# Performance work log

Measured on AMD Instinct MI355X. Metric: run time of the kernel, lower is better.

## Reference

```python
import jax, jax.numpy as jnp
import numpy as np


def _resize_bilinear_ac(img, out_h, out_w):
    """Bilinear resize with align_corners=True. img: [B, C, Hin, Win]."""
    B, C, Hin, Win = img.shape
    ys = jnp.linspace(0.0, Hin - 1.0, out_h)
    xs = jnp.linspace(0.0, Win - 1.0, out_w)
    y0 = jnp.floor(ys).astype(jnp.int32)
    x0 = jnp.floor(xs).astype(jnp.int32)
    y1 = jnp.clip(y0 + 1, 0, Hin - 1)
    x1 = jnp.clip(x0 + 1, 0, Win - 1)
    wy = (ys - y0.astype(ys.dtype))[:, None]   # [out_h, 1]
    wx = (xs - x0.astype(xs.dtype))[None, :]   # [1, out_w]
    g = lambda yi, xi: img[:, :, yi[:, None], xi[None, :]]  # [B,C,out_h,out_w]
    top = (1.0 - wx) * g(y0, x0) + wx * g(y0, x1)
    bot = (1.0 - wx) * g(y1, x0) + wx * g(y1, x1)
    return (1.0 - wy) * top + wy * bot


def setup_inputs() -> dict:
    key = jax.random.key(0)
    k1, k2, k3, k4 = jax.random.split(key, 4)
    B, C, H, W = 4, 2048, 48, 48
    x = jax.random.normal(k1, (B, C, H, W), jnp.float32)
    cam = jax.random.normal(k2, (B, 384, 384), jnp.float32)
    # xavier-uniform 1x1 conv weights: bound = sqrt(6/(fan_in+fan_out))
    bound = float(np.sqrt(6.0 / (C + C)))
    Wq = jax.random.uniform(k3, (C, C), jnp.float32, -bound, bound)
    Wk = jax.random.uniform(k4, (C, C), jnp.float32, -bound, bound)
    bq = jnp.zeros((C,), jnp.float32)
    bk = jnp.zeros((C,), jnp.float32)
    gamma = jnp.ones((1,), jnp.float32)
    return {"x": x, "cam": cam, "Wq": Wq, "bq": bq, "Wk": Wk, "bk": bk, "gamma": gamma}


def reference(x, cam, Wq, bq, Wk, bk, gamma):
    B, C, H, W = x.shape
    N = H * W
    # cam[cam == 255] = 0
    cam = jnp.where(cam == 255.0, 0.0, cam)
    cam_r = _resize_bilinear_ac(cam[:, None, :, :], H, W)      # [B,1,H,W]
    mask = (cam_r > 0).astype(x.dtype).reshape(B, 1, N).transpose(0, 2, 1)  # [B,N,1]
    # 1x1 convs == per-pixel matmul over channels
    q = jnp.einsum('bchw,oc->bohw', x, Wq) + bq[None, :, None, None]
    k = jnp.einsum('bchw,oc->bohw', x, Wk) + bk[None, :, None, None]
    q = q.reshape(B, C, N).transpose(0, 2, 1)   # [B,N,C]
    k = k.reshape(B, C, N)                       # [B,C,N]
    energy = jnp.einsum('bnc,bcm->bnm', q, k)    # [B,N,N]
    q_norm = jnp.sqrt(jnp.sum(q * q, axis=-1, keepdims=True))  # [B,N,1]
    k_norm = jnp.sqrt(jnp.sum(k * k, axis=1, keepdims=True))   # [B,1,N]
    atten = jax.nn.softmax(energy / (q_norm * k_norm), axis=-1)
    atten = mask * atten                         # mask query rows post-softmax
    x_flat = x.reshape(B, C, N)
    new_x = jnp.einsum('bnm,bcm->bcn', atten, x_flat).reshape(B, C, H, W)
    new_x = gamma[0] * new_x
    r = (x - new_x) ** 2
    loss = jnp.sum(r) / jnp.count_nonzero(r).astype(x.dtype)
    return loss
```

## Files before the change

kernel.cpp:

```cpp
#include <hip/hip_runtime.h>
#include <cstdint>
#include <cstddef>

#define BB 4
#define CC 2048
#define HH 48
#define WW 48
#define NN 2304
#define CAMS 384

typedef unsigned short ushort_t;
typedef float f32x4 __attribute__((ext_vector_type(4)));
typedef long longx2 __attribute__((ext_vector_type(2)));

__device__ __forceinline__ ushort_t f2bf(float f) {
    uint32_t u = __builtin_bit_cast(uint32_t, f);
    u += 0x7FFFu + ((u >> 16) & 1u);
    return (ushort_t)(u >> 16);
}
__device__ __forceinline__ float bf2f(ushort_t u) {
    return __builtin_bit_cast(float, (uint32_t)u << 16);
}

__device__ __forceinline__ uint32_t pk2fp8(float a, float b) {
    return (uint32_t)__builtin_amdgcn_cvt_pk_fp8_f32(a, b, 0, false) & 0xFFFFu;
}
__device__ __forceinline__ uint8_t f2fp8(float v) {
    return (uint8_t)(pk2fp8(v, v) & 0xFFu);
}

__device__ __forceinline__ void gld16(const void* g, void* l) {
    __builtin_amdgcn_global_load_lds(
        (const __attribute__((address_space(1))) uint32_t*)g,
        (__attribute__((address_space(3))) uint32_t*)l, 16, 0, 0);
}

__device__ __forceinline__ void mfma_mainloop_fp8(
    const uint8_t* __restrict__ A, const uint8_t* __restrict__ B, int K,
    int m0, int n0, uint8_t* sA, uint8_t* sB, f32x4 acc[4][4])
{
    const int t = threadIdx.x;
    const int lane = t & 63;
    const int w = t >> 6;
    const int wm = (w >> 1) * 64;
    const int wn = (w & 1) * 64;
    const int col = lane & 15;
    const int quad = lane >> 4;
    const int lr = lane >> 2;
    const int lp = lane & 3;

    for (int k0 = 0; k0 < K; k0 += 64) {
        __syncthreads();
        #pragma unroll
        for (int it = 0; it < 2; it++) {
            const int rg = w * 32 + it * 16;
            const int r = rg + lr;
            const int c = lp ^ (r & 3);
            gld16(A + (size_t)(m0 + r) * K + k0 + c * 16, sA + rg * 64);
            gld16(B + (size_t)(n0 + r) * K + k0 + c * 16, sB + rg * 64);
        }
        __syncthreads();
        longx2 af[4], bfr[4];
        #pragma unroll
        for (int i = 0; i < 4; i++) {
            const int m = wm + i * 16 + col;
            af[i] = *(const longx2*)(sA + m * 64 + (quad ^ (m & 3)) * 16);
        }
        #pragma unroll
        for (int j = 0; j < 4; j++) {
            const int n = wn + j * 16 + col;
            bfr[j] = *(const longx2*)(sB + n * 64 + (quad ^ (n & 3)) * 16);
        }
        #pragma unroll
        for (int i = 0; i < 4; i++)
            #pragma unroll
            for (int j = 0; j < 4; j++) {
                acc[i][j] = __builtin_amdgcn_mfma_f32_16x16x32_fp8_fp8(
                    af[i].x, bfr[j].x, acc[i][j], 0, 0, 0);
                acc[i][j] = __builtin_amdgcn_mfma_f32_16x16x32_fp8_fp8(
                    af[i].y, bfr[j].y, acc[i][j], 0, 0, 0);
            }
    }
}

__global__ void init_kernel(float* __restrict__ qn2, float* __restrict__ kn2,
                            float* __restrict__ accf) {
    int t = blockIdx.x * 256 + threadIdx.x;
    if (t < BB * NN) { qn2[t] = 0.f; kn2[t] = 0.f; }
    if (t == 0) { ((double*)accf)[0] = 0.0; ((unsigned int*)accf)[2] = 0u; }
}

__global__ void conv_w(const float* __restrict__ Wq, const float* __restrict__ Wk,
                       uint8_t* __restrict__ Wq8, uint8_t* __restrict__ Wk8) {
    const int per = CC * CC / 4;
    int idx = blockIdx.x * 256 + threadIdx.x;
    if (idx >= 2 * per) return;
    const float4* src; uint8_t* dst; int i;
    if (idx < per) { src = (const float4*)Wq; dst = Wq8; i = idx; }
    else           { src = (const float4*)Wk; dst = Wk8; i = idx - per; }
    float4 v = src[i];
    *(uint32_t*)(dst + (size_t)i * 4) = pk2fp8(v.x, v.y) | (pk2fp8(v.z, v.w) << 16);
}

__global__ void conv_x(const float* __restrict__ x, uint8_t* __restrict__ x8,
                       uint8_t* __restrict__ xT8) {
    __shared__ float tile[32][33];
    const int b = blockIdx.z;
    const int c0 = blockIdx.y * 32, n0 = blockIdx.x * 32;
    const int t = threadIdx.x;
    {
        const int c = t >> 3, n4 = (t & 7) * 4;
        const float4 v = *(const float4*)(x + ((size_t)b * CC + c0 + c) * NN + n0 + n4);
        *(uint32_t*)(x8 + ((size_t)b * CC + c0 + c) * NN + n0 + n4) =
            pk2fp8(v.x, v.y) | (pk2fp8(v.z, v.w) << 16);
        tile[c][n4] = v.x; tile[c][n4 + 1] = v.y;
        tile[c][n4 + 2] = v.z; tile[c][n4 + 3] = v.w;
    }
    __syncthreads();
    {
        const int n = t >> 3, c4 = (t & 7) * 4;
        uint32_t u = pk2fp8(tile[c4][n], tile[c4 + 1][n])
                   | (pk2fp8(tile[c4 + 2][n], tile[c4 + 3][n]) << 16);
        *(uint32_t*)(xT8 + ((size_t)b * NN + n0 + n) * CC + c0 + c4) = u;
    }
}

__global__ __launch_bounds__(256) void gemm_proj(
    const uint8_t* __restrict__ xT8,
    const uint8_t* __restrict__ Wq8, const uint8_t* __restrict__ Wk8,
    const float* __restrict__ bq, const float* __restrict__ bk,
    uint8_t* __restrict__ qT8, uint8_t* __restrict__ kT8,
    float* __restrict__ qn2, float* __restrict__ kn2)
{
    __shared__ __align__(16) uint8_t sA[128 * 64];
    __shared__ __align__(16) uint8_t sB[128 * 64];
    const int z = blockIdx.z;
    const int b = z >> 1, which = z & 1;
    const uint8_t* Wb   = which ? Wk8 : Wq8;
    const float*   bias = which ? bk  : bq;
    uint8_t*       outT = which ? kT8 : qT8;
    float*         nrm  = which ? kn2 : qn2;
    const int m0 = blockIdx.y * 128;
    const int n0 = blockIdx.x * 128;
    f32x4 acc[4][4];
    const f32x4 zz = {0.f, 0.f, 0.f, 0.f};
    #pragma unroll
    for (int i = 0; i < 4; i++)
        #pragma unroll
        for (int j = 0; j < 4; j++) acc[i][j] = zz;
    mfma_mainloop_fp8(xT8 + (size_t)b * NN * CC, Wb, CC, m0, n0, sA, sB, acc);
    const int t = threadIdx.x, lane = t & 63, w = t >> 6;
    const int wm = (w >> 1) * 64, wn = (w & 1) * 64;
    const int col = lane & 15, quad = lane >> 4;
    uint8_t* O = outT + (size_t)b * NN * CC;
    float sq[4][4];
    #pragma unroll
    for (int i = 0; i < 4; i++)
        #pragma unroll
        for (int r = 0; r < 4; r++) sq[i][r] = 0.f;
    #pragma unroll
    for (int j = 0; j < 4; j++) {
        const int gn = n0 + wn + j * 16 + col;
        const float bv = bias[gn];
        #pragma unroll
        for (int i = 0; i < 4; i++) {
            const int gm = m0 + wm + i * 16 + quad * 4;
            #pragma unroll
            for (int r = 0; r < 4; r++) {
                float v = acc[i][j][r] + bv;
                O[(size_t)(gm + r) * CC + gn] = f2fp8(v);
                sq[i][r] += v * v;
            }
        }
    }
    #pragma unroll
    for (int i = 0; i < 4; i++)
        #pragma unroll
        for (int r = 0; r < 4; r++) {
            float s = sq[i][r];
            #pragma unroll
            for (int o = 1; o < 16; o <<= 1) s += __shfl_xor(s, o, 64);
            if (col == 0) {
                const int gm = m0 + wm + i * 16 + quad * 4 + r;
                atomicAdd(&nrm[b * NN + gm], s);
            }
        }
}

__global__ __launch_bounds__(256) void gemm_energy(
    const uint8_t* __restrict__ qT8, const uint8_t* __restrict__ kT8,
    ushort_t* __restrict__ S)
{
    __shared__ __align__(16) uint8_t sA[128 * 64];
    __shared__ __align__(16) uint8_t sB[128 * 64];
    const int b = blockIdx.z;
    const int m0 = blockIdx.y * 128;
    const int n0 = blockIdx.x * 128;
    f32x4 acc[4][4];
    const f32x4 zz = {0.f, 0.f, 0.f, 0.f};
    #pragma unroll
    for (int i = 0; i < 4; i++)
        #pragma unroll
        for (int j = 0; j < 4; j++) acc[i][j] = zz;
    mfma_mainloop_fp8(qT8 + (size_t)b * NN * CC, kT8 + (size_t)b * NN * CC, CC,
                      m0, n0, sA, sB, acc);
    const int t = threadIdx.x, lane = t & 63, w = t >> 6;
    const int wm = (w >> 1) * 64, wn = (w & 1) * 64;
    const int col = lane & 15, quad = lane >> 4;
    ushort_t* O = S + (size_t)b * NN * NN;
    #pragma unroll
    for (int i = 0; i < 4; i++) {
        const int gm = m0 + wm + i * 16 + quad * 4;
        #pragma unroll
        for (int j = 0; j < 4; j++) {
            const int gn = n0 + wn + j * 16 + col;
            #pragma unroll
            for (int r = 0; r < 4; r++)
                O[(size_t)(gm + r) * NN + gn] = f2bf(acc[i][j][r]);
        }
    }
}

__global__ __launch_bounds__(256) void softmax_kernel(
    const ushort_t* __restrict__ S, uint8_t* __restrict__ att,
    const float* __restrict__ qn2, const float* __restrict__ kn2,
    const float* __restrict__ cam)
{
    const int n = blockIdx.x, b = blockIdx.y;
    const ushort_t* row = S + ((size_t)b * NN + n) * NN;
    uint8_t* orow = att + ((size_t)b * NN + n) * NN;
    const float qinv = rsqrtf(qn2[b * NN + n]);
    const int y = n / WW, xx = n % WW;
    const float ys = (float)(y  * (CAMS - 1)) / (float)(HH - 1);
    const float xs = (float)(xx * (CAMS - 1)) / (float)(WW - 1);
    const int y0 = (int)ys, x0 = (int)xs;
    const int y1 = min(y0 + 1, CAMS - 1), x1 = min(x0 + 1, CAMS - 1);
    const float wy = ys - (float)y0, wx = xs - (float)x0;
    const float* cb = cam + (size_t)b * CAMS * CAMS;
    float c00 = cb[y0 * CAMS + x0]; if (c00 == 255.f) c00 = 0.f;
    float c01 = cb[y0 * CAMS + x1]; if (c01 == 255.f) c01 = 0.f;
    float c10 = cb[y1 * CAMS + x0]; if (c10 == 255.f) c10 = 0.f;
    float c11 = cb[y1 * CAMS + x1]; if (c11 == 255.f) c11 = 0.f;
    const float mv = (1.f - wy) * ((1.f - wx) * c00 + wx * c01)
                   +        wy  * ((1.f - wx) * c10 + wx * c11);
    const float mval = (mv > 0.f) ? 1.f : 0.f;

    const int t = threadIdx.x;
    float v[9];
    float vmax = -3.4e38f;
    #pragma unroll
    for (int i = 0; i < 9; i++) {
        int idx = t + i * 256;
        float s = bf2f(row[idx]) * qinv * rsqrtf(kn2[b * NN + idx]);
        v[i] = s;
        vmax = fmaxf(vmax, s);
    }
    __shared__ float red[8];
    int lane = t & 63, wid = t >> 6;
    #pragma unroll
    for (int o = 32; o; o >>= 1) vmax = fmaxf(vmax, __shfl_down(vmax, o, 64));
    if (!lane) red[wid] = vmax;
    __syncthreads();
    vmax = fmaxf(fmaxf(red[0], red[1]), fmaxf(red[2], red[3]));
    float s = 0.f;
    #pragma unroll
    for (int i = 0; i < 9; i++) { v[i] = __expf(v[i] - vmax); s += v[i]; }
    #pragma unroll
    for (int o = 32; o; o >>= 1) s += __shfl_down(s, o, 64);
    if (!lane) red[4 + wid] = s;
    __syncthreads();
    s = red[4] + red[5] + red[6] + red[7];
    const float scale = mval * 256.f / s;
    #pragma unroll
    for (int i = 0; i < 9; i++) orow[t + i * 256] = f2fp8(v[i] * scale);
}

__global__ __launch_bounds__(256) void gemm_out_loss(
    const uint8_t* __restrict__ x8, const uint8_t* __restrict__ att,
    const float* __restrict__ x, const float* __restrict__ gamma,
    float* __restrict__ accf)
{
    __shared__ __align__(16) uint8_t sA[128 * 64];
    __shared__ __align__(16) uint8_t sB[128 * 64];
    const int b = blockIdx.z;
    const int m0 = blockIdx.y * 128;
    const int n0 = blockIdx.x * 128;
    f32x4 acc[4][4];
    const f32x4 zz = {0.f, 0.f, 0.f, 0.f};
    #pragma unroll
    for (int i = 0; i < 4; i++)
        #pragma unroll
        for (int j = 0; j < 4; j++) acc[i][j] = zz;
    mfma_mainloop_fp8(x8 + (size_t)b * CC * NN, att + (size_t)b * NN * NN, NN,
                      m0, n0, sA, sB, acc);
    const int t = threadIdx.x, lane = t & 63, w = t >> 6;
    const int wm = (w >> 1) * 64, wn = (w & 1) * 64;
    const int col = lane & 15, quad = lane >> 4;
    const float g = gamma[0] * (1.f / 256.f);
    const float* Xb = x + (size_t)b * CC * NN;
    float lsum = 0.f;
    unsigned int lcnt = 0;
    #pragma unroll
    for (int i = 0; i < 4; i++) {
        const int gm = m0 + wm + i * 16 + quad * 4;
        #pragma unroll
        for (int j = 0; j < 4; j++) {
            const int gn = n0 + wn + j * 16 + col;
            #pragma unroll
            for (int r = 0; r < 4; r++) {
                float xv = Xb[(size_t)(gm + r) * NN + gn];
                float d = xv - g * acc[i][j][r];
                float r2 = d * d;
                lsum += r2;
                lcnt += (r2 != 0.f) ? 1u : 0u;
            }
        }
    }
    #pragma unroll
    for (int o = 32; o; o >>= 1) {
        lsum += __shfl_down(lsum, o, 64);
        lcnt += __shfl_down(lcnt, o, 64);
    }
    __shared__ float rs[4];
    __shared__ unsigned int rc[4];
    if (!lane) { rs[w] = lsum; rc[w] = lcnt; }
    __syncthreads();
    if (t == 0) {
        double tot = (double)rs[0] + rs[1] + rs[2] + rs[3];
        unsigned int ct = rc[0] + rc[1] + rc[2] + rc[3];
        atomicAdd((double*)accf, tot);
        atomicAdd(((unsigned int*)accf) + 2, ct);
    }
}

__global__ void finalize_kernel(const float* __restrict__ accf, float* __restrict__ out) {
    double s = ((const double*)accf)[0];
    unsigned int c = ((const unsigned int*)accf)[2];
    out[0] = (float)(s / (double)c);
}

extern "C" void kernel_launch(void* const* d_in, const int* in_sizes, int n_in,
                              void* d_out, int out_size, void* d_ws, size_t ws_size,
                              hipStream_t stream) {
    const float* x     = (const float*)d_in[0];
    const float* cam   = (const float*)d_in[1];
    const float* Wq    = (const float*)d_in[2];
    const float* bq    = (const float*)d_in[3];
    const float* Wk    = (const float*)d_in[4];
    const float* bk    = (const float*)d_in[5];
    const float* gamma = (const float*)d_in[6];

    uint8_t* ws = (uint8_t*)d_ws;
    size_t off = 0;
    auto alloc = [&](size_t bytes) {
        void* p = ws + off;
        off = (off + bytes + 255) & ~(size_t)255;
        return p;
    };
    uint8_t*  qT8  = (uint8_t*)alloc((size_t)BB * NN * CC);
    uint8_t*  kT8  = (uint8_t*)alloc((size_t)BB * NN * CC);
    uint8_t*  xT8  = (uint8_t*)alloc((size_t)BB * NN * CC);
    uint8_t*  x8   = (uint8_t*)alloc((size_t)BB * CC * NN);
    uint8_t*  att  = (uint8_t*)alloc((size_t)BB * NN * NN);
    ushort_t* S    = (ushort_t*)alloc((size_t)BB * NN * NN * 2);
    uint8_t*  Wq8  = (uint8_t*)alloc((size_t)CC * CC);
    uint8_t*  Wk8  = (uint8_t*)alloc((size_t)CC * CC);
    float*    qn2  = (float*)alloc((size_t)BB * NN * 4);
    float*    kn2  = (float*)alloc((size_t)BB * NN * 4);
    float*    acc  = (float*)alloc(16);

    hipLaunchKernelGGL(init_kernel, dim3((BB * NN + 255) / 256), dim3(256), 0, stream,
                       qn2, kn2, acc);
    hipLaunchKernelGGL(conv_w, dim3(2 * CC * CC / 4 / 256), dim3(256), 0, stream,
                       Wq, Wk, Wq8, Wk8);
    hipLaunchKernelGGL(conv_x, dim3(NN / 32, CC / 32, BB), dim3(256), 0, stream,
                       x, x8, xT8);
    hipLaunchKernelGGL(gemm_proj, dim3(CC / 128, NN / 128, BB * 2), dim3(256), 0, stream,
                       xT8, Wq8, Wk8, bq, bk, qT8, kT8, qn2, kn2);
    hipLaunchKernelGGL(gemm_energy, dim3(NN / 128, NN / 128, BB), dim3(256), 0, stream,
                       qT8, kT8, S);
    hipLaunchKernelGGL(softmax_kernel, dim3(NN, BB), dim3(256), 0, stream,
                       S, att, qn2, kn2, cam);
    hipLaunchKernelGGL(gemm_out_loss, dim3(NN / 128, CC / 128, BB), dim3(256), 0, stream,
                       x8, att, x, gamma, acc);
    hipLaunchKernelGGL(finalize_kernel, dim3(1), dim3(1), 0, stream, acc, (float*)d_out);
}
```

Measured before the change: 497.1 us.

## Switch FP8 GEMM mainloop to MX-scaled 16x16x128 MFMA with K=128 tiles

Replaces the pair of 16x16x32 fp8 MFMAs per k-step with the gfx950 scaled 16x16x128 f8f6f4 MFMA using a unit scale, and doubles the K tile to 128. The LDS tiles grow to 128x128 bytes each, with an 8-way XOR swizzle, and each lane loads 32 bytes per fragment. The aim is higher MFMA throughput and half as many loop iterations and barriers, at the cost of more LDS per block, which may lower occupancy, plus the risk that the operand layout or scale encoding is wrong.

```diff
diff --git a/kernel.cpp b/kernel.cpp
--- a/kernel.cpp
+++ b/kernel.cpp
@@ -11,7 +11,10 @@
 
 typedef unsigned short ushort_t;
 typedef float f32x4 __attribute__((ext_vector_type(4)));
-typedef long longx2 __attribute__((ext_vector_type(2)));
+typedef int i32x4 __attribute__((ext_vector_type(4)));
+typedef int i32x8 __attribute__((ext_vector_type(8)));
+
+#define SCALE1 0x7F7F7F7F
 
 __device__ __forceinline__ ushort_t f2bf(float f) {
     uint32_t u = __builtin_bit_cast(uint32_t, f);
@@ -35,7 +38,7 @@
         (__attribute__((address_space(3))) uint32_t*)l, 16, 0, 0);
 }
 
-__device__ __forceinline__ void mfma_mainloop_fp8(
+__device__ __forceinline__ void mfma_mainloop_mx(
     const uint8_t* __restrict__ A, const uint8_t* __restrict__ B, int K,
     int m0, int n0, uint8_t* sA, uint8_t* sB, f32x4 acc[4][4])
 {
@@ -46,40 +49,40 @@
     const int wn = (w & 1) * 64;
     const int col = lane & 15;
     const int quad = lane >> 4;
-    const int lr = lane >> 2;
-    const int lp = lane & 3;
-
-    for (int k0 = 0; k0 < K; k0 += 64) {
+    const int lr = lane >> 3;
+    const int lp = lane & 7;
+
+    for (int k0 = 0; k0 < K; k0 += 128) {
         __syncthreads();
         #pragma unroll
-        for (int it = 0; it < 2; it++) {
-            const int rg = w * 32 + it * 16;
+        for (int it = 0; it < 4; it++) {
+            const int rg = w * 32 + it * 8;
             const int r = rg + lr;
-            const int c = lp ^ (r & 3);
-            gld16(A + (size_t)(m0 + r) * K + k0 + c * 16, sA + rg * 64);
-            gld16(B + (size_t)(n0 + r) * K + k0 + c * 16, sB + rg * 64);
+            const int c = lp ^ (r & 7);
+            gld16(A + (size_t)(m0 + r) * K + k0 + c * 16, sA + rg * 128);
+            gld16(B + (size_t)(n0 + r) * K + k0 + c * 16, sB + rg * 128);
         }
         __syncthreads();
-        longx2 af[4], bfr[4];
+        i32x8 bfr[4];
+        #pragma unroll
+        for (int j = 0; j < 4; j++) {
+            const int n = wn + j * 16 + col;
+            i32x4 lo = *(const i32x4*)(sB + n * 128 + ((2 * quad) ^ (n & 7)) * 16);
+            i32x4 hi = *(const i32x4*)(sB + n * 128 + ((2 * quad + 1) ^ (n & 7)) * 16);
+            bfr[j] = (i32x8){lo.x, lo.y, lo.z, lo.w, hi.x, hi.y, hi.z, hi.w};
+        }
         #pragma unroll
         for (int i = 0; i < 4; i++) {
             const int m = wm + i * 16 + col;
-            af[i] = *(const longx2*)(sA + m * 64 + (quad ^ (m & 3)) * 16);
-        }
-        #pragma unroll
-        for (int j = 0; j < 4; j++) {
-            const int n = wn + j * 16 + col;
-            bfr[j] = *(const longx2*)(sB + n * 64 + (quad ^ (n & 3)) * 16);
-        }
-        #pragma unroll
-        for (int i = 0; i < 4; i++)
-            #pragma unroll
-            for (int j = 0; j < 4; j++) {
-                acc[i][j] = __builtin_amdgcn_mfma_f32_16x16x32_fp8_fp8(
-                    af[i].x, bfr[j].x, acc[i][j], 0, 0, 0);
-                acc[i][j] = __builtin_amdgcn_mfma_f32_16x16x32_fp8_fp8(
-                    af[i].y, bfr[j].y, acc[i][j], 0, 0, 0);
-            }
+            i32x4 lo = *(const i32x4*)(sA + m * 128 + ((2 * quad) ^ (m & 7)) * 16);
+            i32x4 hi = *(const i32x4*)(sA + m * 128 + ((2 * quad + 1) ^ (m & 7)) * 16);
+            i32x8 af = (i32x8){lo.x, lo.y, lo.z, lo.w, hi.x, hi.y, hi.z, hi.w};
+            #pragma unroll
+            for (int j = 0; j < 4; j++)
+                acc[i][j] = __builtin_amdgcn_mfma_scale_f32_16x16x128_f8f6f4(
+                    af, bfr[j], acc[i][j], 0, 0,
+                    0, SCALE1, 0, SCALE1);
+        }
     }
 }
 
@@ -132,8 +135,8 @@
     uint8_t* __restrict__ qT8, uint8_t* __restrict__ kT8,
     float* __restrict__ qn2, float* __restrict__ kn2)
 {
-    __shared__ __align__(16) uint8_t sA[128 * 64];
-    __shared__ __align__(16) uint8_t sB[128 * 64];
+    __shared__ __align__(16) uint8_t sA[128 * 128];
+    __shared__ __align__(16) uint8_t sB[128 * 128];
     const int z = blockIdx.z;
     const int b = z >> 1, which = z & 1;
     const uint8_t* Wb   = which ? Wk8 : Wq8;
@@ -148,7 +151,7 @@
     for (int i = 0; i < 4; i++)
         #pragma unroll
         for (int j = 0; j < 4; j++) acc[i][j] = zz;
-    mfma_mainloop_fp8(xT8 + (size_t)b * NN * CC, Wb, CC, m0, n0, sA, sB, acc);
+    mfma_mainloop_mx(xT8 + (size_t)b * NN * CC, Wb, CC, m0, n0, sA, sB, acc);
     const int t = threadIdx.x, lane = t & 63, w = t >> 6;
     const int wm = (w >> 1) * 64, wn = (w & 1) * 64;
     const int col = lane & 15, quad = lane >> 4;
@@ -191,8 +194,8 @@
     const uint8_t* __restrict__ qT8, const uint8_t* __restrict__ kT8,
     ushort_t* __restrict__ S)
 {
-    __shared__ __align__(16) uint8_t sA[128 * 64];
-    __shared__ __align__(16) uint8_t sB[128 * 64];
+    __shared__ __align__(16) uint8_t sA[128 * 128];
+    __shared__ __align__(16) uint8_t sB[128 * 128];
     const int b = blockIdx.z;
     const int m0 = blockIdx.y * 128;
     const int n0 = blockIdx.x * 128;
@@ -202,8 +205,8 @@
     for (int i = 0; i < 4; i++)
         #pragma unroll
         for (int j = 0; j < 4; j++) acc[i][j] = zz;
-    mfma_mainloop_fp8(qT8 + (size_t)b * NN * CC, kT8 + (size_t)b * NN * CC, CC,
-                      m0, n0, sA, sB, acc);
+    mfma_mainloop_mx(qT8 + (size_t)b * NN * CC, kT8 + (size_t)b * NN * CC, CC,
+                     m0, n0, sA, sB, acc);
     const int t = threadIdx.x, lane = t & 63, w = t >> 6;
     const int wm = (w >> 1) * 64, wn = (w & 1) * 64;
     const int col = lane & 15, quad = lane >> 4;
@@ -280,8 +283,8 @@
     const float* __restrict__ x, const float* __restrict__ gamma,
     float* __restrict__ accf)
 {
-    __shared__ __align__(16) uint8_t sA[128 * 64];
-    __shared__ __align__(16) uint8_t sB[128 * 64];
+    __shared__ __align__(16) uint8_t sA[128 * 128];
+    __shared__ __align__(16) uint8_t sB[128 * 128];
     const int b = blockIdx.z;
     const int m0 = blockIdx.y * 128;
     const int n0 = blockIdx.x * 128;
@@ -291,8 +294,8 @@
     for (int i = 0; i < 4; i++)
         #pragma unroll
         for (int j = 0; j < 4; j++) acc[i][j] = zz;
-    mfma_mainloop_fp8(x8 + (size_t)b * CC * NN, att + (size_t)b * NN * NN, NN,
-                      m0, n0, sA, sB, acc);
+    mfma_mainloop_mx(x8 + (size_t)b * CC * NN, att + (size_t)b * NN * NN, NN,
+                     m0, n0, sA, sB, acc);
     const int t = threadIdx.x, lane = t & 63, w = t >> 6;
     const int wm = (w >> 1) * 64, wn = (w & 1) * 64;
     const int col = lane & 15, quad = lane >> 4;
```

Result: faster. 431.9 us (-13.1%).
